# Kernel optimization log

Measured on AMD Instinct MI355X. Metric: run time of the kernel, lower is better.

## Reference

```python
import jax, jax.numpy as jnp
import numpy as np

B, N, NPOINT, NSAMPLE = 8, 4096, 1024, 32
IN_CH = 29
MLP = [64, 64, 128]
D_IN = IN_CH + 3  # 32
D_OUT = 128
EPS = 1e-5


def setup_inputs() -> dict:
    key = jax.random.key(0)
    ks = jax.random.split(key, 32)
    inp = {}
    inp["xyz"] = jax.random.normal(ks[0], (B, 3, N), jnp.float32)
    inp["points"] = jax.random.normal(ks[1], (B, IN_CH, N), jnp.float32)
    last = IN_CH + 3
    for i, oc in enumerate(MLP):
        inp[f"mlp_w{i}"] = jax.random.normal(ks[2 + i], (oc, last), jnp.float32) * np.sqrt(2.0 / last).astype(np.float32)
        inp[f"mlp_b{i}"] = jnp.zeros((oc,), jnp.float32)
        inp[f"mlp_g{i}"] = jnp.ones((oc,), jnp.float32)
        inp[f"mlp_be{i}"] = jnp.zeros((oc,), jnp.float32)
        last = oc
    inp["conv1_w"] = jax.random.normal(ks[10], (D_OUT // 2, 4), jnp.float32) * np.float32(np.sqrt(2.0 / 4))
    inp["conv1_b"] = jnp.zeros((D_OUT // 2,), jnp.float32)
    inp["bn1_g"] = jnp.ones((D_OUT // 2,), jnp.float32)
    inp["bn1_be"] = jnp.zeros((D_OUT // 2,), jnp.float32)
    inp["conv2_w"] = jax.random.normal(ks[11], (D_OUT // 2, D_IN), jnp.float32) * np.float32(np.sqrt(2.0 / D_IN))
    inp["conv2_b"] = jnp.zeros((D_OUT // 2,), jnp.float32)
    inp["bn2_g"] = jnp.ones((D_OUT // 2,), jnp.float32)
    inp["bn2_be"] = jnp.zeros((D_OUT // 2,), jnp.float32)
    return inp


def _conv1x1(x, w, b):
    # x: [B,Cin,ns,S], w: [Cout,Cin] -> [B,Cout,ns,S]
    return jnp.einsum("bcns,oc->bons", x, w) + b[None, :, None, None]


def _bn_relu(x, g, be):
    # training-mode BatchNorm2d: batch stats over (B, ns, S), biased variance
    m = jnp.mean(x, axis=(0, 2, 3), keepdims=True)
    v = jnp.var(x, axis=(0, 2, 3), keepdims=True)
    y = g[None, :, None, None] * (x - m) * jax.lax.rsqrt(v + EPS) + be[None, :, None, None]
    return jax.nn.relu(y)


def _fps(xyz):
    # xyz: [B,N,3] -> centroid indices [B,NPOINT]; deterministic start at index 0
    Bn, Nn, _ = xyz.shape

    def step(carry, _):
        dist, far = carry
        cen = jnp.take_along_axis(xyz, far[:, None, None], axis=1)  # [B,1,3]
        d = jnp.sum((xyz - cen) ** 2, axis=-1)                      # [B,N]
        dist = jnp.minimum(dist, d)
        new_far = jnp.argmax(dist, axis=-1).astype(jnp.int32)
        return (dist, new_far), far

    init = (jnp.full((Bn, Nn), 1e10, xyz.dtype), jnp.zeros((Bn,), jnp.int32))
    _, cents = jax.lax.scan(step, init, None, length=NPOINT)
    return cents.T  # [B,NPOINT]


def _forward(xyz, points, mlp_params, conv1_w, conv1_b, bn1_g, bn1_be,
             conv2_w, conv2_b, bn2_g, bn2_be):
    xyz_t = xyz.transpose(0, 2, 1)      # [B,N,3]
    pts_t = points.transpose(0, 2, 1)   # [B,N,C]
    xyz_sg = jax.lax.stop_gradient(xyz_t)

    ct_idx = _fps(xyz_sg)                                   # [B,S]
    bidx = jnp.arange(B)[:, None]
    ct_xyz = xyz_t[bidx, ct_idx]                            # [B,S,3]

    # kNN via squared distances (indices only -> stop_gradient)
    ct_sg = jax.lax.stop_gradient(ct_xyz)
    d2 = (jnp.sum(ct_sg ** 2, -1)[:, :, None]
          + jnp.sum(xyz_sg ** 2, -1)[:, None, :]
          - 2.0 * jnp.einsum("bsc,bnc->bsn", ct_sg, xyz_sg))  # [B,S,N]
    _, gidx = jax.lax.top_k(-d2, NSAMPLE)                     # [B,S,ns]

    bidx3 = jnp.arange(B)[:, None, None]
    grouped_xyz = xyz_t[bidx3, gidx]                          # [B,S,ns,3]
    ft_xyz = grouped_xyz - ct_xyz[:, :, None, :]              # [B,S,ns,3]
    ft_points = jnp.concatenate([ft_xyz, pts_t[bidx3, gidx]], axis=-1)  # [B,S,ns,3+C]
    ft = ft_points.transpose(0, 3, 2, 1)                      # [B,3+C,ns,S]

    # shared MLP (conv-bn-relu stack), then max over neighbors
    x = ft
    for (w, b, g, be) in mlp_params:
        x = _bn_relu(_conv1x1(x, w, b), g, be)
    new_points1 = jnp.max(x, axis=2)                          # [B,mlp[-1],S]

    # relative positional encoding branch
    ct_p = ct_xyz.transpose(0, 2, 1)                          # [B,3,S]
    grouped_p = grouped_xyz.transpose(0, 3, 2, 1)             # [B,3,ns,S]
    rel = grouped_p - ct_p[:, :, None, :]                     # [B,3,ns,S]
    rd = jnp.sqrt(jnp.maximum(jnp.sum(rel ** 2, axis=1, keepdims=True), 1e-12))
    new_xyz = _bn_relu(_conv1x1(jnp.concatenate([rel, rd], axis=1), conv1_w, conv1_b), bn1_g, bn1_be)
    new_pts = _bn_relu(_conv1x1(ft, conv2_w, conv2_b), bn2_g, bn2_be)

    f_concat = jnp.concatenate([new_xyz, new_pts], axis=1)    # [B,d_out,ns,S]
    new_points2 = jnp.concatenate([jnp.mean(f_concat, axis=2), jnp.max(f_concat, axis=2)], axis=1)
    conv_points = jnp.concatenate([new_points1, new_points2], axis=1)  # [B,mlp[-1]+2*d_out,S]
    return ct_p, conv_points


def reference(xyz, points,
              mlp_w0, mlp_b0, mlp_g0, mlp_be0,
              mlp_w1, mlp_b1, mlp_g1, mlp_be1,
              mlp_w2, mlp_b2, mlp_g2, mlp_be2,
              conv1_w, conv1_b, bn1_g, bn1_be,
              conv2_w, conv2_b, bn2_g, bn2_be):
    mlp_params = [(mlp_w0, mlp_b0, mlp_g0, mlp_be0),
                  (mlp_w1, mlp_b1, mlp_g1, mlp_be1),
                  (mlp_w2, mlp_b2, mlp_g2, mlp_be2)]
    return _forward(xyz, points, mlp_params, conv1_w, conv1_b, bn1_g, bn1_be,
                    conv2_w, conv2_b, bn2_g, bn2_be)
```

## Files before the change

kernel.cpp:

```cpp
#include <hip/hip_runtime.h>
#include <cfloat>
#include <math.h>

constexpr int B_ = 8, N_ = 4096, S_ = 1024, NS_ = 32;
constexpr int R_ = B_ * S_ * NS_;
constexpr float EPS_ = 1e-5f;

__device__ __forceinline__ unsigned dpp_red_umax(unsigned x) {
    unsigned t;
#define STEP_(ctrl) t = (unsigned)__builtin_amdgcn_update_dpp((int)x, (int)x, ctrl, 0xf, 0xf, false); x = x > t ? x : t;
    STEP_(0x111) STEP_(0x112) STEP_(0x114) STEP_(0x118) STEP_(0x142) STEP_(0x143)
#undef STEP_
    return x;
}
__device__ __forceinline__ unsigned dpp_red_umin(unsigned x) {
    unsigned t;
#define STEP_(ctrl) t = (unsigned)__builtin_amdgcn_update_dpp((int)x, (int)x, ctrl, 0xf, 0xf, false); x = x < t ? x : t;
    STEP_(0x111) STEP_(0x112) STEP_(0x114) STEP_(0x118) STEP_(0x142) STEP_(0x143)
#undef STEP_
    return x;
}
__device__ __forceinline__ void dpp_min_u64(unsigned& hi, unsigned& lo) {
#define STEP_(ctrl) { \
    unsigned h2 = (unsigned)__builtin_amdgcn_update_dpp((int)hi, (int)hi, ctrl, 0xf, 0xf, false); \
    unsigned l2 = (unsigned)__builtin_amdgcn_update_dpp((int)lo, (int)lo, ctrl, 0xf, 0xf, false); \
    if (h2 < hi || (h2 == hi && l2 < lo)) { hi = h2; lo = l2; } }
    STEP_(0x111) STEP_(0x112) STEP_(0x114) STEP_(0x118) STEP_(0x142) STEP_(0x143)
#undef STEP_
}
__device__ __forceinline__ float dpp_sum_f32(float x) {
#define ADD_(ctrl, rm) { \
    int t_ = __builtin_amdgcn_update_dpp(0, __float_as_int(x), ctrl, rm, 0xf, true); \
    x += __int_as_float(t_); }
    ADD_(0x111, 0xf) ADD_(0x112, 0xf) ADD_(0x114, 0xf) ADD_(0x118, 0xf)
    ADD_(0x142, 0xa) ADD_(0x143, 0xc)
#undef ADD_
    return x;
}

__global__ __launch_bounds__(256) void fps_kernel(const float* __restrict__ xyz,
                                                  int* __restrict__ ct_idx) {
    int b = blockIdx.x;
    const float* xb = xyz + (size_t)b * 3 * N_;
    int t = threadIdx.x;
    __shared__ float4 sp[N_];
    __shared__ int sct[S_];
    __shared__ unsigned long long sb[2][4];
    for (int i = t; i < N_; i += 256) {
        float x = xb[i], y = xb[N_ + i], z = xb[2 * N_ + i];
        sp[i] = make_float4(x, y, z, 0.f);
    }
    float px[16], py[16], pz[16], dist[16];
    unsigned idxr[16];
#pragma unroll
    for (int j = 0; j < 16; j++) {
        int n = j * 256 + t;
        px[j] = xb[n];
        py[j] = xb[N_ + n];
        pz[j] = xb[2 * N_ + n];
        dist[j] = 1e10f;
        idxr[j] = (unsigned)n;
    }
    __syncthreads();
    float4 c4 = sp[0];
    int far = 0;
    int w = t >> 6;
    for (int it = 0; it < S_; it++) {
        if (t == 0) sct[it] = far;
#pragma unroll
        for (int j = 0; j < 16; j++) {
            float dx = px[j] - c4.x, dy = py[j] - c4.y, dz = pz[j] - c4.z;
            float d = dx * dx;
            d = fmaf(dy, dy, d);
            d = fmaf(dz, dz, d);
            dist[j] = fminf(dist[j], d);
        }
        float v8[8], v4[4];
#pragma unroll
        for (int j = 0; j < 8; j++) v8[j] = fmaxf(dist[2 * j], dist[2 * j + 1]);
#pragma unroll
        for (int j = 0; j < 4; j++) v4[j] = fmaxf(v8[2 * j], v8[2 * j + 1]);
        float lmax = fmaxf(fmaxf(v4[0], v4[1]), fmaxf(v4[2], v4[3]));
        unsigned wm = (unsigned)__builtin_amdgcn_readlane(
            (int)dpp_red_umax(__float_as_uint(lmax)), 63);
        unsigned c8[8], c4i[4];
#pragma unroll
        for (int j = 0; j < 8; j++) {
            unsigned a = (__float_as_uint(dist[2 * j]) == wm) ? idxr[2 * j] : 0xffffffffu;
            unsigned bq = (__float_as_uint(dist[2 * j + 1]) == wm) ? idxr[2 * j + 1] : 0xffffffffu;
            c8[j] = a < bq ? a : bq;
        }
#pragma unroll
        for (int j = 0; j < 4; j++) c4i[j] = c8[2 * j] < c8[2 * j + 1] ? c8[2 * j] : c8[2 * j + 1];
        unsigned c01 = c4i[0] < c4i[1] ? c4i[0] : c4i[1];
        unsigned c23 = c4i[2] < c4i[3] ? c4i[2] : c4i[3];
        unsigned mn = dpp_red_umin(c01 < c23 ? c01 : c23);
        int p = it & 1;
        if ((t & 63) == 63)
            sb[p][w] = ((unsigned long long)wm << 32) | (unsigned)~mn;
        __syncthreads();
        unsigned long long b0 = sb[p][0], b1 = sb[p][1], b2 = sb[p][2], b3 = sb[p][3];
        unsigned long long ma = b0 > b1 ? b0 : b1;
        unsigned long long mb = b2 > b3 ? b2 : b3;
        unsigned long long bw = ma > mb ? ma : mb;
        far = (int)(~(unsigned)(bw & 0xffffffffu)) & (N_ - 1);
        c4 = sp[far];
    }
    __syncthreads();
    for (int i = t; i < S_; i += 256) ct_idx[b * S_ + i] = sct[i];
}

__global__ __launch_bounds__(256) void knn_kernel(const float* __restrict__ xyz,
                                                  const int* __restrict__ ct_idx,
                                                  int* __restrict__ gidx) {
    int bs = blockIdx.x;
    int b = bs >> 10;
    const float* xb = xyz + (size_t)b * 3 * N_;
    int ci = ct_idx[bs];
    float cx = xb[ci], cy = xb[N_ + ci], cz = xb[2 * N_ + ci];
    float cs = cx * cx + cy * cy + cz * cz;
    int t = threadIdx.x;
    unsigned long long pk[16];
#pragma unroll
    for (int j = 0; j < 16; j++) {
        int n = j * 256 + t;
        float x = xb[n], y = xb[N_ + n], z = xb[2 * N_ + n];
        float xn = x * x + y * y + z * z;
        float dot = cx * x + cy * y + cz * z;
        float val = cs + xn - 2.f * dot;
        unsigned vb = __float_as_uint(val);
        unsigned key = (vb & 0x80000000u) ? ~vb : (vb | 0x80000000u);
        pk[j] = ((unsigned long long)key << 32) | (unsigned)n;
    }
    __shared__ unsigned long long sw[2][4];
    int out_base = bs * NS_;
    int w = t >> 6;
    for (int iter = 0; iter < NS_; iter++) {
        unsigned long long m8[8], m4[4];
#pragma unroll
        for (int j = 0; j < 8; j++) m8[j] = pk[2 * j] < pk[2 * j + 1] ? pk[2 * j] : pk[2 * j + 1];
#pragma unroll
        for (int j = 0; j < 4; j++) m4[j] = m8[2 * j] < m8[2 * j + 1] ? m8[2 * j] : m8[2 * j + 1];
        unsigned long long ma = m4[0] < m4[1] ? m4[0] : m4[1];
        unsigned long long mb = m4[2] < m4[3] ? m4[2] : m4[3];
        unsigned long long best = ma < mb ? ma : mb;
        unsigned hi = (unsigned)(best >> 32), lo = (unsigned)best;
        dpp_min_u64(hi, lo);
        int p = iter & 1;
        if ((t & 63) == 63) sw[p][w] = ((unsigned long long)hi << 32) | lo;
        __syncthreads();
        unsigned long long b0 = sw[p][0], b1 = sw[p][1], b2 = sw[p][2], b3 = sw[p][3];
        unsigned long long wa = b0 < b1 ? b0 : b1;
        unsigned long long wb = b2 < b3 ? b2 : b3;
        unsigned long long bw = wa < wb ? wa : wb;
        int n = (int)(unsigned)(bw & 0xffffffffu);
        if (t == 0) gidx[out_base + iter] = n;
        if ((n & 255) == t) pk[n >> 8] = 0xFFFFFFFF00000000ull | (unsigned)n;
    }
}

__global__ __launch_bounds__(256) void ctp_kernel(const float* __restrict__ xyz,
                                                  const int* __restrict__ ct_idx,
                                                  float* __restrict__ out) {
    int i = blockIdx.x * 256 + threadIdx.x;
    if (i >= B_ * 3 * S_) return;
    int b = i / (3 * S_);
    int rem = i - b * 3 * S_;
    int c = rem >> 10;
    int s = rem & (S_ - 1);
    int ci = ct_idx[b * S_ + s];
    out[i] = xyz[(size_t)b * 3 * N_ + (size_t)c * N_ + ci];
}

__global__ __launch_bounds__(256) void gather_kernel(const float* __restrict__ xyz,
                                                     const float* __restrict__ pts,
                                                     const int* __restrict__ ct_idx,
                                                     const int* __restrict__ gidx,
                                                     float* __restrict__ ft) {
    int r = blockIdx.x * 256 + threadIdx.x;
    int b = r >> 15;
    int s = (r >> 5) & (S_ - 1);
    int g = gidx[r];
    int ci = ct_idx[b * S_ + s];
    const float* xb = xyz + (size_t)b * 3 * N_;
    float rx = xb[g] - xb[ci];
    float ry = xb[N_ + g] - xb[N_ + ci];
    float rz = xb[2 * N_ + g] - xb[2 * N_ + ci];
    ft[r] = rx;
    ft[(size_t)R_ + r] = ry;
    ft[(size_t)2 * R_ + r] = rz;
    float rd = sqrtf(fmaxf(rx * rx + ry * ry + rz * rz, 1e-12f));
    ft[(size_t)32 * R_ + r] = rd;
    const float* pb = pts + (size_t)b * 29 * N_;
#pragma unroll
    for (int c = 0; c < 29; c++) ft[(size_t)(3 + c) * R_ + r] = pb[(size_t)c * N_ + g];
}

template <int CIN, bool AFF>
__global__ __launch_bounds__(256) void convk(const float* __restrict__ xin,
                                             const float* __restrict__ W,
                                             const float* __restrict__ bias,
                                             const float* __restrict__ ab,
                                             float* __restrict__ out0,
                                             float* __restrict__ out1,
                                             float* __restrict__ partial) {
    __shared__ float Ws[CIN][64];
    __shared__ float bs_[64];
    __shared__ float as_[CIN], bbs[CIN];
    __shared__ float red[4][64][2];
    int oc0 = blockIdx.y * 64;
    for (int i = threadIdx.x; i < CIN * 64; i += 256) {
        int o = i & 63, c = i >> 6;
        Ws[c][o] = W[(size_t)(oc0 + o) * CIN + c];
    }
    if (threadIdx.x < 64) bs_[threadIdx.x] = bias[oc0 + threadIdx.x];
    if (AFF) {
        for (int i = threadIdx.x; i < CIN; i += 256) { as_[i] = ab[i]; bbs[i] = ab[CIN + i]; }
    }
    __syncthreads();
    size_t r0 = (size_t)blockIdx.x * 512 + threadIdx.x;
    float acc0[64], acc1[64];
#pragma unroll
    for (int o = 0; o < 64; o++) { acc0[o] = 0.f; acc1[o] = 0.f; }
    for (int c = 0; c < CIN; c++) {
        float x0 = xin[(size_t)c * R_ + r0];
        float x1 = xin[(size_t)c * R_ + r0 + 256];
        if (AFF) {
            float a = as_[c], bb = bbs[c];
            x0 = fmaxf(fmaf(a, x0, bb), 0.f);
            x1 = fmaxf(fmaf(a, x1, bb), 0.f);
        }
#pragma unroll
        for (int o = 0; o < 64; o++) {
            float w = Ws[c][o];
            acc0[o] = fmaf(x0, w, acc0[o]);
            acc1[o] = fmaf(x1, w, acc1[o]);
        }
    }
    float* outp = blockIdx.y ? out1 : out0;
    int wv = threadIdx.x >> 6;
#pragma unroll
    for (int o = 0; o < 64; o++) {
        float bv = bs_[o];
        float y0 = acc0[o] + bv;
        float y1 = acc1[o] + bv;
        outp[(size_t)o * R_ + r0] = y0;
        outp[(size_t)o * R_ + r0 + 256] = y1;
        float s = y0 + y1;
        float q = fmaf(y0, y0, y1 * y1);
        s = dpp_sum_f32(s);
        q = dpp_sum_f32(q);
        if ((threadIdx.x & 63) == 63) { red[wv][o][0] = s; red[wv][o][1] = q; }
    }
    __syncthreads();
    if (threadIdx.x < 64) {
        int o = threadIdx.x;
        float s = red[0][o][0] + red[1][o][0] + red[2][o][0] + red[3][o][0];
        float q = red[0][o][1] + red[1][o][1] + red[2][o][1] + red[3][o][1];
        partial[(size_t)(oc0 + o) * 1024 + blockIdx.x] = s;
        partial[(size_t)(oc0 + o) * 1024 + 512 + blockIdx.x] = q;
    }
}

__global__ __launch_bounds__(256) void conv1_kernel(const float* __restrict__ ft,
                                                    const float* __restrict__ W,
                                                    const float* __restrict__ bias,
                                                    float* __restrict__ out,
                                                    float* __restrict__ partial) {
    __shared__ float Ws[4][64];
    __shared__ float bs_[64];
    __shared__ float red[4][64][2];
    {
        int i = threadIdx.x;
        if (i < 256) { int o = i & 63, c = i >> 6; Ws[c][o] = W[o * 4 + c]; }
    }
    if (threadIdx.x < 64) bs_[threadIdx.x] = bias[threadIdx.x];
    __syncthreads();
    size_t r0 = (size_t)blockIdx.x * 512 + threadIdx.x;
    float acc0[64], acc1[64];
#pragma unroll
    for (int o = 0; o < 64; o++) { acc0[o] = 0.f; acc1[o] = 0.f; }
    const int chs[4] = {0, 1, 2, 32};
#pragma unroll
    for (int c = 0; c < 4; c++) {
        int ch = chs[c];
        float x0 = ft[(size_t)ch * R_ + r0];
        float x1 = ft[(size_t)ch * R_ + r0 + 256];
#pragma unroll
        for (int o = 0; o < 64; o++) {
            float w = Ws[c][o];
            acc0[o] = fmaf(x0, w, acc0[o]);
            acc1[o] = fmaf(x1, w, acc1[o]);
        }
    }
    int wv = threadIdx.x >> 6;
#pragma unroll
    for (int o = 0; o < 64; o++) {
        float bv = bs_[o];
        float y0 = acc0[o] + bv;
        float y1 = acc1[o] + bv;
        out[(size_t)o * R_ + r0] = y0;
        out[(size_t)o * R_ + r0 + 256] = y1;
        float s = y0 + y1;
        float q = fmaf(y0, y0, y1 * y1);
        s = dpp_sum_f32(s);
        q = dpp_sum_f32(q);
        if ((threadIdx.x & 63) == 63) { red[wv][o][0] = s; red[wv][o][1] = q; }
    }
    __syncthreads();
    if (threadIdx.x < 64) {
        int o = threadIdx.x;
        float s = red[0][o][0] + red[1][o][0] + red[2][o][0] + red[3][o][0];
        float q = red[0][o][1] + red[1][o][1] + red[2][o][1] + red[3][o][1];
        partial[(size_t)o * 1024 + blockIdx.x] = s;
        partial[(size_t)o * 1024 + 512 + blockIdx.x] = q;
    }
}

__global__ __launch_bounds__(64) void statsf(const float* __restrict__ partial,
                                             const float* __restrict__ g,
                                             const float* __restrict__ be,
                                             float* __restrict__ ab, int C) {
    int c = blockIdx.x, t = threadIdx.x;
    float s = 0.f, q = 0.f;
    for (int i = t; i < 512; i += 64) {
        s += partial[(size_t)c * 1024 + i];
        q += partial[(size_t)c * 1024 + 512 + i];
    }
    s = dpp_sum_f32(s);
    q = dpp_sum_f32(q);
    if (t == 63) {
        float inv = 1.0f / (float)R_;
        float mean = s * inv;
        float var = q * inv - mean * mean;
        float a = g[c] / sqrtf(var + EPS_);
        ab[c] = a;
        ab[C + c] = be[c] - mean * a;
    }
}

__global__ __launch_bounds__(128) void final_max(const float* __restrict__ yA,
                                                 const float* __restrict__ yC,
                                                 const float* __restrict__ ab,
                                                 float* __restrict__ out) {
    int bs = blockIdx.x;
    int c = threadIdx.x;
    const float* src = (c < 64 ? yA + (size_t)c * R_ : yC + (size_t)(c - 64) * R_) + (size_t)bs * NS_;
    float a = ab[c], bb = ab[128 + c];
    const float4* s4 = reinterpret_cast<const float4*>(src);
    float m = -FLT_MAX;
#pragma unroll
    for (int i = 0; i < 8; i++) {
        float4 v = s4[i];
        m = fmaxf(m, fmaxf(fmaf(a, v.x, bb), 0.f));
        m = fmaxf(m, fmaxf(fmaf(a, v.y, bb), 0.f));
        m = fmaxf(m, fmaxf(fmaf(a, v.z, bb), 0.f));
        m = fmaxf(m, fmaxf(fmaf(a, v.w, bb), 0.f));
    }
    int b = bs >> 10, s = bs & (S_ - 1);
    out[24576 + (size_t)b * 393216 + (size_t)c * 1024 + s] = m;
}

__global__ __launch_bounds__(128) void final_meanmax(const float* __restrict__ z1,
                                                     const float* __restrict__ z2,
                                                     const float* __restrict__ ab1,
                                                     const float* __restrict__ ab2,
                                                     float* __restrict__ out) {
    int bs = blockIdx.x;
    int c = threadIdx.x;
    const float* src;
    float a, bb;
    if (c < 64) { src = z1 + (size_t)c * R_; a = ab1[c]; bb = ab1[64 + c]; }
    else        { src = z2 + (size_t)(c - 64) * R_; a = ab2[c - 64]; bb = ab2[64 + (c - 64)]; }
    src += (size_t)bs * NS_;
    const float4* s4 = reinterpret_cast<const float4*>(src);
    float m = -FLT_MAX, sm = 0.f;
#pragma unroll
    for (int i = 0; i < 8; i++) {
        float4 v = s4[i];
        float t0 = fmaxf(fmaf(a, v.x, bb), 0.f); sm += t0; m = fmaxf(m, t0);
        float t1 = fmaxf(fmaf(a, v.y, bb), 0.f); sm += t1; m = fmaxf(m, t1);
        float t2 = fmaxf(fmaf(a, v.z, bb), 0.f); sm += t2; m = fmaxf(m, t2);
        float t3 = fmaxf(fmaf(a, v.w, bb), 0.f); sm += t3; m = fmaxf(m, t3);
    }
    int b = bs >> 10, s = bs & (S_ - 1);
    size_t ob = 24576 + (size_t)b * 393216;
    out[ob + (size_t)(128 + c) * 1024 + s] = sm * 0.03125f;
    out[ob + (size_t)(256 + c) * 1024 + s] = m;
}

extern "C" void kernel_launch(void* const* d_in, const int* in_sizes, int n_in,
                              void* d_out, int out_size, void* d_ws, size_t ws_size,
                              hipStream_t stream) {
    const float* xyz = (const float*)d_in[0];
    const float* pts = (const float*)d_in[1];
    const float* W0 = (const float*)d_in[2];  const float* b0 = (const float*)d_in[3];
    const float* g0 = (const float*)d_in[4];  const float* be0 = (const float*)d_in[5];
    const float* W1 = (const float*)d_in[6];  const float* b1 = (const float*)d_in[7];
    const float* g1 = (const float*)d_in[8];  const float* be1 = (const float*)d_in[9];
    const float* W2 = (const float*)d_in[10]; const float* b2 = (const float*)d_in[11];
    const float* g2 = (const float*)d_in[12]; const float* be2 = (const float*)d_in[13];
    const float* c1w = (const float*)d_in[14]; const float* c1b = (const float*)d_in[15];
    const float* bg1 = (const float*)d_in[16]; const float* bbe1 = (const float*)d_in[17];
    const float* c2w = (const float*)d_in[18]; const float* c2b = (const float*)d_in[19];
    const float* bg2 = (const float*)d_in[20]; const float* bbe2 = (const float*)d_in[21];
    float* out = (float*)d_out;

    int* ct_idx = (int*)d_ws;
    int* gidx = ct_idx + B_ * S_;
    float* fbase = (float*)d_ws;
    float* ft = fbase + 270336;
    float* A = ft + (size_t)33 * R_;
    float* Bb = A + (size_t)64 * R_;
    float* C = Bb + (size_t)64 * R_;
    float* partial = C + (size_t)64 * R_;
    float* ab0 = partial + 131072;
    float* ab1 = ab0 + 128;
    float* ab2 = ab1 + 128;
    float* abz1 = ab2 + 256;
    float* abz2 = abz1 + 128;

    fps_kernel<<<B_, 256, 0, stream>>>(xyz, ct_idx);
    knn_kernel<<<B_ * S_, 256, 0, stream>>>(xyz, ct_idx, gidx);
    ctp_kernel<<<(B_ * 3 * S_ + 255) / 256, 256, 0, stream>>>(xyz, ct_idx, out);
    gather_kernel<<<R_ / 256, 256, 0, stream>>>(xyz, pts, ct_idx, gidx, ft);

    convk<32, false><<<dim3(R_ / 512, 1), 256, 0, stream>>>(ft, W0, b0, nullptr, A, nullptr, partial);
    statsf<<<64, 64, 0, stream>>>(partial, g0, be0, ab0, 64);
    convk<64, true><<<dim3(R_ / 512, 1), 256, 0, stream>>>(A, W1, b1, ab0, Bb, nullptr, partial);
    statsf<<<64, 64, 0, stream>>>(partial, g1, be1, ab1, 64);
    convk<64, true><<<dim3(R_ / 512, 2), 256, 0, stream>>>(Bb, W2, b2, ab1, A, C, partial);
    statsf<<<128, 64, 0, stream>>>(partial, g2, be2, ab2, 128);
    final_max<<<B_ * S_, 128, 0, stream>>>(A, C, ab2, out);

    convk<32, false><<<dim3(R_ / 512, 1), 256, 0, stream>>>(ft, c2w, c2b, nullptr, Bb, nullptr, partial);
    statsf<<<64, 64, 0, stream>>>(partial, bg2, bbe2, abz2, 64);

    conv1_kernel<<<R_ / 512, 256, 0, stream>>>(ft, c1w, c1b, A, partial);
    statsf<<<64, 64, 0, stream>>>(partial, bg1, bbe1, abz1, 64);

    final_meanmax<<<B_ * S_, 128, 0, stream>>>(A, Bb, abz1, abz2, out);
}
```

Measured before the change: 1.467 ms.

## Fuse BN stats into conv prologues, transpose points for gather, pack FPS math

```diff
diff --git a/kernel.cpp b/kernel.cpp
--- a/kernel.cpp
+++ b/kernel.cpp
@@ -5,6 +5,8 @@
 constexpr int B_ = 8, N_ = 4096, S_ = 1024, NS_ = 32;
 constexpr int R_ = B_ * S_ * NS_;
 constexpr float EPS_ = 1e-5f;
+
+typedef float v2f __attribute__((ext_vector_type(2)));
 
 __device__ __forceinline__ unsigned dpp_red_umax(unsigned x) {
     unsigned t;
@@ -38,60 +40,78 @@
     return x;
 }
 
+__global__ __launch_bounds__(256) void transpose_kernel(const float* __restrict__ xyz,
+                                                        const float* __restrict__ pts,
+                                                        float* __restrict__ ptsT) {
+    int idx = blockIdx.x * 256 + threadIdx.x;
+    int b = idx >> 12, n = idx & (N_ - 1);
+    float* row = ptsT + (size_t)idx * 32;
+    const float* pb = pts + (size_t)b * 29 * N_;
+#pragma unroll
+    for (int c = 0; c < 29; c++) row[c] = pb[(size_t)c * N_ + n];
+    const float* xb = xyz + (size_t)b * 3 * N_;
+    row[29] = xb[n];
+    row[30] = xb[N_ + n];
+    row[31] = xb[2 * N_ + n];
+}
+
 __global__ __launch_bounds__(256) void fps_kernel(const float* __restrict__ xyz,
                                                   int* __restrict__ ct_idx) {
     int b = blockIdx.x;
     const float* xb = xyz + (size_t)b * 3 * N_;
     int t = threadIdx.x;
-    __shared__ float4 sp[N_];
-    __shared__ int sct[S_];
+    __shared__ float sx[N_], sy[N_], sz[N_];
     __shared__ unsigned long long sb[2][4];
     for (int i = t; i < N_; i += 256) {
-        float x = xb[i], y = xb[N_ + i], z = xb[2 * N_ + i];
-        sp[i] = make_float4(x, y, z, 0.f);
-    }
-    float px[16], py[16], pz[16], dist[16];
-    unsigned idxr[16];
-#pragma unroll
-    for (int j = 0; j < 16; j++) {
-        int n = j * 256 + t;
-        px[j] = xb[n];
-        py[j] = xb[N_ + n];
-        pz[j] = xb[2 * N_ + n];
-        dist[j] = 1e10f;
-        idxr[j] = (unsigned)n;
+        sx[i] = xb[i];
+        sy[i] = xb[N_ + i];
+        sz[i] = xb[2 * N_ + i];
+    }
+    v2f px[8], py[8], pz[8], dist[8];
+#pragma unroll
+    for (int k = 0; k < 8; k++) {
+        int n0 = (2 * k) * 256 + t, n1 = (2 * k + 1) * 256 + t;
+        px[k] = (v2f){xb[n0], xb[n1]};
+        py[k] = (v2f){xb[N_ + n0], xb[N_ + n1]};
+        pz[k] = (v2f){xb[2 * N_ + n0], xb[2 * N_ + n1]};
+        dist[k] = (v2f){1e10f, 1e10f};
     }
     __syncthreads();
-    float4 c4 = sp[0];
+    float cx = sx[0], cy = sy[0], cz = sz[0];
     int far = 0;
     int w = t >> 6;
     for (int it = 0; it < S_; it++) {
-        if (t == 0) sct[it] = far;
-#pragma unroll
-        for (int j = 0; j < 16; j++) {
-            float dx = px[j] - c4.x, dy = py[j] - c4.y, dz = pz[j] - c4.z;
-            float d = dx * dx;
-            d = fmaf(dy, dy, d);
-            d = fmaf(dz, dz, d);
-            dist[j] = fminf(dist[j], d);
-        }
-        float v8[8], v4[4];
-#pragma unroll
-        for (int j = 0; j < 8; j++) v8[j] = fmaxf(dist[2 * j], dist[2 * j + 1]);
-#pragma unroll
-        for (int j = 0; j < 4; j++) v4[j] = fmaxf(v8[2 * j], v8[2 * j + 1]);
-        float lmax = fmaxf(fmaxf(v4[0], v4[1]), fmaxf(v4[2], v4[3]));
+        if (t == 0) ct_idx[b * S_ + it] = far;
+        v2f cx2 = (v2f){cx, cx}, cy2 = (v2f){cy, cy}, cz2 = (v2f){cz, cz};
+#pragma unroll
+        for (int k = 0; k < 8; k++) {
+            v2f dx = px[k] - cx2, dy = py[k] - cy2, dz = pz[k] - cz2;
+            v2f d = dx * dx;
+            d = __builtin_elementwise_fma(dy, dy, d);
+            d = __builtin_elementwise_fma(dz, dz, d);
+            dist[k] = __builtin_elementwise_min(dist[k], d);
+        }
+        v2f m4[4];
+#pragma unroll
+        for (int k = 0; k < 4; k++)
+            m4[k] = __builtin_elementwise_max(dist[2 * k], dist[2 * k + 1]);
+        v2f m2a = __builtin_elementwise_max(m4[0], m4[1]);
+        v2f m2b = __builtin_elementwise_max(m4[2], m4[3]);
+        v2f m1 = __builtin_elementwise_max(m2a, m2b);
+        float lmax = fmaxf(m1.x, m1.y);
         unsigned wm = (unsigned)__builtin_amdgcn_readlane(
             (int)dpp_red_umax(__float_as_uint(lmax)), 63);
         unsigned c8[8], c4i[4];
 #pragma unroll
-        for (int j = 0; j < 8; j++) {
-            unsigned a = (__float_as_uint(dist[2 * j]) == wm) ? idxr[2 * j] : 0xffffffffu;
-            unsigned bq = (__float_as_uint(dist[2 * j + 1]) == wm) ? idxr[2 * j + 1] : 0xffffffffu;
-            c8[j] = a < bq ? a : bq;
-        }
-#pragma unroll
-        for (int j = 0; j < 4; j++) c4i[j] = c8[2 * j] < c8[2 * j + 1] ? c8[2 * j] : c8[2 * j + 1];
+        for (int k = 0; k < 8; k++) {
+            unsigned a = (__float_as_uint(dist[k].x) == wm)
+                             ? (unsigned)((2 * k) * 256 + t) : 0xffffffffu;
+            unsigned bq = (__float_as_uint(dist[k].y) == wm)
+                             ? (unsigned)((2 * k + 1) * 256 + t) : 0xffffffffu;
+            c8[k] = a < bq ? a : bq;
+        }
+#pragma unroll
+        for (int k = 0; k < 4; k++) c4i[k] = c8[2 * k] < c8[2 * k + 1] ? c8[2 * k] : c8[2 * k + 1];
         unsigned c01 = c4i[0] < c4i[1] ? c4i[0] : c4i[1];
         unsigned c23 = c4i[2] < c4i[3] ? c4i[2] : c4i[3];
         unsigned mn = dpp_red_umin(c01 < c23 ? c01 : c23);
@@ -104,10 +124,8 @@
         unsigned long long mb = b2 > b3 ? b2 : b3;
         unsigned long long bw = ma > mb ? ma : mb;
         far = (int)(~(unsigned)(bw & 0xffffffffu)) & (N_ - 1);
-        c4 = sp[far];
-    }
-    __syncthreads();
-    for (int i = t; i < S_; i += 256) ct_idx[b * S_ + i] = sct[i];
+        cx = sx[far]; cy = sy[far]; cz = sz[far];
+    }
 }
 
 __global__ __launch_bounds__(256) void knn_kernel(const float* __restrict__ xyz,
@@ -159,51 +177,56 @@
     }
 }
 
-__global__ __launch_bounds__(256) void ctp_kernel(const float* __restrict__ xyz,
-                                                  const int* __restrict__ ct_idx,
-                                                  float* __restrict__ out) {
-    int i = blockIdx.x * 256 + threadIdx.x;
-    if (i >= B_ * 3 * S_) return;
-    int b = i / (3 * S_);
-    int rem = i - b * 3 * S_;
-    int c = rem >> 10;
-    int s = rem & (S_ - 1);
-    int ci = ct_idx[b * S_ + s];
-    out[i] = xyz[(size_t)b * 3 * N_ + (size_t)c * N_ + ci];
-}
-
-__global__ __launch_bounds__(256) void gather_kernel(const float* __restrict__ xyz,
-                                                     const float* __restrict__ pts,
+__global__ __launch_bounds__(256) void gather_kernel(const float* __restrict__ ptsT,
+                                                     const float* __restrict__ xyz,
                                                      const int* __restrict__ ct_idx,
                                                      const int* __restrict__ gidx,
-                                                     float* __restrict__ ft) {
+                                                     float* __restrict__ ft,
+                                                     float* __restrict__ out) {
     int r = blockIdx.x * 256 + threadIdx.x;
     int b = r >> 15;
     int s = (r >> 5) & (S_ - 1);
     int g = gidx[r];
     int ci = ct_idx[b * S_ + s];
-    const float* xb = xyz + (size_t)b * 3 * N_;
-    float rx = xb[g] - xb[ci];
-    float ry = xb[N_ + g] - xb[N_ + ci];
-    float rz = xb[2 * N_ + g] - xb[2 * N_ + ci];
+    const float4* rowg = (const float4*)(ptsT + ((size_t)(b << 12) + g) * 32);
+    float4 v[8];
+#pragma unroll
+    for (int i = 0; i < 8; i++) v[i] = rowg[i];
+    float4 cw = ((const float4*)(ptsT + ((size_t)(b << 12) + ci) * 32))[7];
+    float rx = v[7].y - cw.y;
+    float ry = v[7].z - cw.z;
+    float rz = v[7].w - cw.w;
     ft[r] = rx;
     ft[(size_t)R_ + r] = ry;
     ft[(size_t)2 * R_ + r] = rz;
     float rd = sqrtf(fmaxf(rx * rx + ry * ry + rz * rz, 1e-12f));
     ft[(size_t)32 * R_ + r] = rd;
-    const float* pb = pts + (size_t)b * 29 * N_;
-#pragma unroll
-    for (int c = 0; c < 29; c++) ft[(size_t)(3 + c) * R_ + r] = pb[(size_t)c * N_ + g];
-}
-
-template <int CIN, bool AFF>
+    const float vals[32] = {v[0].x, v[0].y, v[0].z, v[0].w, v[1].x, v[1].y, v[1].z, v[1].w,
+                            v[2].x, v[2].y, v[2].z, v[2].w, v[3].x, v[3].y, v[3].z, v[3].w,
+                            v[4].x, v[4].y, v[4].z, v[4].w, v[5].x, v[5].y, v[5].z, v[5].w,
+                            v[6].x, v[6].y, v[6].z, v[6].w, v[7].x, 0.f, 0.f, 0.f};
+#pragma unroll
+    for (int c = 0; c < 29; c++) ft[(size_t)(3 + c) * R_ + r] = vals[c];
+    if (r < B_ * 3 * S_) {
+        int bb = r / (3 * S_);
+        int rem = r - bb * 3 * S_;
+        int cc = rem >> 10;
+        int ss = rem & (S_ - 1);
+        int cidx = ct_idx[bb * S_ + ss];
+        out[r] = xyz[(size_t)bb * 3 * N_ + (size_t)cc * N_ + cidx];
+    }
+}
+
+template <int CIN, bool PRO>
 __global__ __launch_bounds__(256) void convk(const float* __restrict__ xin,
                                              const float* __restrict__ W,
                                              const float* __restrict__ bias,
-                                             const float* __restrict__ ab,
+                                             const float* __restrict__ pread,
+                                             const float* __restrict__ g,
+                                             const float* __restrict__ be,
+                                             float* __restrict__ pwrite, int pofs,
                                              float* __restrict__ out0,
-                                             float* __restrict__ out1,
-                                             float* __restrict__ partial) {
+                                             float* __restrict__ out1) {
     __shared__ float Ws[CIN][64];
     __shared__ float bs_[64];
     __shared__ float as_[CIN], bbs[CIN];
@@ -214,8 +237,21 @@
         Ws[c][o] = W[(size_t)(oc0 + o) * CIN + c];
     }
     if (threadIdx.x < 64) bs_[threadIdx.x] = bias[oc0 + threadIdx.x];
-    if (AFF) {
-        for (int i = threadIdx.x; i < CIN; i += 256) { as_[i] = ab[i]; bbs[i] = ab[CIN + i]; }
+    if (PRO) {
+        int c = threadIdx.x >> 2, sub = threadIdx.x & 3;
+        const float* ps = pread + (size_t)c * 1024 + sub * 128;
+        float s = 0.f, q = 0.f;
+        for (int i = 0; i < 128; i++) { s += ps[i]; q += ps[512 + i]; }
+        s += __shfl_xor(s, 1); s += __shfl_xor(s, 2);
+        q += __shfl_xor(q, 1); q += __shfl_xor(q, 2);
+        if (sub == 0) {
+            float inv = 1.0f / (float)R_;
+            float mean = s * inv;
+            float var = q * inv - mean * mean;
+            float a = g[c] / sqrtf(var + EPS_);
+            as_[c] = a;
+            bbs[c] = be[c] - mean * a;
+        }
     }
     __syncthreads();
     size_t r0 = (size_t)blockIdx.x * 512 + threadIdx.x;
@@ -225,7 +261,7 @@
     for (int c = 0; c < CIN; c++) {
         float x0 = xin[(size_t)c * R_ + r0];
         float x1 = xin[(size_t)c * R_ + r0 + 256];
-        if (AFF) {
+        if (PRO) {
             float a = as_[c], bb = bbs[c];
             x0 = fmaxf(fmaf(a, x0, bb), 0.f);
             x1 = fmaxf(fmaf(a, x1, bb), 0.f);
@@ -257,8 +293,8 @@
         int o = threadIdx.x;
         float s = red[0][o][0] + red[1][o][0] + red[2][o][0] + red[3][o][0];
         float q = red[0][o][1] + red[1][o][1] + red[2][o][1] + red[3][o][1];
-        partial[(size_t)(oc0 + o) * 1024 + blockIdx.x] = s;
-        partial[(size_t)(oc0 + o) * 1024 + 512 + blockIdx.x] = q;
+        pwrite[(size_t)(pofs + oc0 + o) * 1024 + blockIdx.x] = s;
+        pwrite[(size_t)(pofs + oc0 + o) * 1024 + 512 + blockIdx.x] = q;
     }
 }
 
@@ -266,7 +302,7 @@
                                                     const float* __restrict__ W,
                                                     const float* __restrict__ bias,
                                                     float* __restrict__ out,
-                                                    float* __restrict__ partial) {
+                                                    float* __restrict__ pwrite, int pofs) {
     __shared__ float Ws[4][64];
     __shared__ float bs_[64];
     __shared__ float red[4][64][2];
@@ -312,8 +348,8 @@
         int o = threadIdx.x;
         float s = red[0][o][0] + red[1][o][0] + red[2][o][0] + red[3][o][0];
         float q = red[0][o][1] + red[1][o][1] + red[2][o][1] + red[3][o][1];
-        partial[(size_t)o * 1024 + blockIdx.x] = s;
-        partial[(size_t)o * 1024 + 512 + blockIdx.x] = q;
+        pwrite[(size_t)(pofs + o) * 1024 + blockIdx.x] = s;
+        pwrite[(size_t)(pofs + o) * 1024 + 512 + blockIdx.x] = q;
     }
 }
 
@@ -336,6 +372,32 @@
         float a = g[c] / sqrtf(var + EPS_);
         ab[c] = a;
         ab[C + c] = be[c] - mean * a;
+    }
+}
+
+__global__ __launch_bounds__(64) void statsf2(const float* __restrict__ partial,
+                                              const float* __restrict__ g1,
+                                              const float* __restrict__ be1,
+                                              const float* __restrict__ g2,
+                                              const float* __restrict__ be2,
+                                              float* __restrict__ ab) {
+    int c = blockIdx.x, t = threadIdx.x;
+    float s = 0.f, q = 0.f;
+    for (int i = t; i < 512; i += 64) {
+        s += partial[(size_t)c * 1024 + i];
+        q += partial[(size_t)c * 1024 + 512 + i];
+    }
+    s = dpp_sum_f32(s);
+    q = dpp_sum_f32(q);
+    if (t == 63) {
+        float gv = c < 64 ? g1[c] : g2[c - 64];
+        float bv = c < 64 ? be1[c] : be2[c - 64];
+        float inv = 1.0f / (float)R_;
+        float mean = s * inv;
+        float var = q * inv - mean * mean;
+        float a = gv / sqrtf(var + EPS_);
+        ab[c] = a;
+        ab[128 + c] = bv - mean * a;
     }
 }
 
@@ -363,16 +425,12 @@
 
 __global__ __launch_bounds__(128) void final_meanmax(const float* __restrict__ z1,
                                                      const float* __restrict__ z2,
-                                                     const float* __restrict__ ab1,
-                                                     const float* __restrict__ ab2,
+                                                     const float* __restrict__ ab,
                                                      float* __restrict__ out) {
     int bs = blockIdx.x;
     int c = threadIdx.x;
-    const float* src;
-    float a, bb;
-    if (c < 64) { src = z1 + (size_t)c * R_; a = ab1[c]; bb = ab1[64 + c]; }
-    else        { src = z2 + (size_t)(c - 64) * R_; a = ab2[c - 64]; bb = ab2[64 + (c - 64)]; }
-    src += (size_t)bs * NS_;
+    const float* src = (c < 64 ? z1 + (size_t)c * R_ : z2 + (size_t)(c - 64) * R_) + (size_t)bs * NS_;
+    float a = ab[c], bb = ab[128 + c];
     const float4* s4 = reinterpret_cast<const float4*>(src);
     float m = -FLT_MAX, sm = 0.f;
 #pragma unroll
@@ -413,31 +471,25 @@
     float* A = ft + (size_t)33 * R_;
     float* Bb = A + (size_t)64 * R_;
     float* C = Bb + (size_t)64 * R_;
-    float* partial = C + (size_t)64 * R_;
-    float* ab0 = partial + 131072;
-    float* ab1 = ab0 + 128;
-    float* ab2 = ab1 + 128;
-    float* abz1 = ab2 + 256;
-    float* abz2 = abz1 + 128;
-
+    float* pbufA = C + (size_t)64 * R_;
+    float* pbufB = pbufA + 131072;
+    float* ab2 = pbufB + 131072;
+    float* abz = ab2 + 256;
+    float* ptsT = A;
+
+    transpose_kernel<<<B_ * N_ / 256, 256, 0, stream>>>(xyz, pts, ptsT);
     fps_kernel<<<B_, 256, 0, stream>>>(xyz, ct_idx);
     knn_kernel<<<B_ * S_, 256, 0, stream>>>(xyz, ct_idx, gidx);
-    ctp_kernel<<<(B_ * 3 * S_ + 255) / 256, 256, 0, stream>>>(xyz, ct_idx, out);
-    gather_kernel<<<R_ / 256, 256, 0, stream>>>(xyz, pts, ct_idx, gidx, ft);
-
-    convk<32, false><<<dim3(R_ / 512, 1), 256, 0, stream>>>(ft, W0, b0, nullptr, A, nullptr, partial);
-    statsf<<<64, 64, 0, stream>>>(partial, g0, be0, ab0, 64);
-    convk<64, true><<<dim3(R_ / 512, 1), 256, 0, stream>>>(A, W1, b1, ab0, Bb, nullptr, partial);
-    statsf<<<64, 64, 0, stream>>>(partial, g1, be1, ab1, 64);
-    convk<64, true><<<dim3(R_ / 512, 2), 256, 0, stream>>>(Bb, W2, b2, ab1, A, C, partial);
-    statsf<<<128, 64, 0, stream>>>(partial, g2, be2, ab2, 128);
+    gather_kernel<<<R_ / 256, 256, 0, stream>>>(ptsT, xyz, ct_idx, gidx, ft, out);
+
+    convk<32, false><<<dim3(R_ / 512, 1), 256, 0, stream>>>(ft, W0, b0, nullptr, nullptr, nullptr, pbufA, 0, A, nullptr);
+    convk<64, true><<<dim3(R_ / 512, 1), 256, 0, stream>>>(A, W1, b1, pbufA, g0, be0, pbufB, 0, Bb, nullptr);
+    convk<64, true><<<dim3(R_ / 512, 2), 256, 0, stream>>>(Bb, W2, b2, pbufB, g1, be1, pbufA, 0, A, C);
+    statsf<<<128, 64, 0, stream>>>(pbufA, g2, be2, ab2, 128);
     final_max<<<B_ * S_, 128, 0, stream>>>(A, C, ab2, out);
 
-    convk<32, false><<<dim3(R_ / 512, 1), 256, 0, stream>>>(ft, c2w, c2b, nullptr, Bb, nullptr, partial);
-    statsf<<<64, 64, 0, stream>>>(partial, bg2, bbe2, abz2, 64);
-
-    conv1_kernel<<<R_ / 512, 256, 0, stream>>>(ft, c1w, c1b, A, partial);
-    statsf<<<64, 64, 0, stream>>>(partial, bg1, bbe1, abz1, 64);
-
-    final_meanmax<<<B_ * S_, 128, 0, stream>>>(A, Bb, abz1, abz2, out);
-}
+    convk<32, false><<<dim3(R_ / 512, 1), 256, 0, stream>>>(ft, c2w, c2b, nullptr, nullptr, nullptr, pbufB, 64, Bb, nullptr);
+    conv1_kernel<<<R_ / 512, 256, 0, stream>>>(ft, c1w, c1b, A, pbufB, 0);
+    statsf2<<<128, 64, 0, stream>>>(pbufB, bg1, bbe1, bg2, bbe2, abz);
+    final_meanmax<<<B_ * S_, 128, 0, stream>>>(A, Bb, abz, out);
+}
```

New measurement: 1.355 ms. 7.6% less time.
